# Performance work log

Hardware: AMD Instinct MI355X
Metric: run time of the kernel (lower is better)

Reference implementation:

```python
import jax, jax.numpy as jnp
import numpy as np

N = 50000   # total nodes across batched graphs
E = 800000  # total edges
F = 30      # input node features
G = 256     # number of graphs in the disjoint batch
CH = [128, 64, 32]
N_LABELS = 2


def setup_inputs() -> dict:
    key = jax.random.key(0)
    ks = jax.random.split(key, 16)
    x = jax.random.normal(ks[0], (N, F), dtype=jnp.float32)
    edge_weight = jax.random.uniform(ks[1], (E,), dtype=jnp.float32)
    edge_row = jax.random.randint(ks[2], (E,), 0, N, dtype=jnp.int32)
    edge_col = jax.random.randint(ks[3], (E,), 0, N, dtype=jnp.int32)
    seg = jnp.sort(jax.random.randint(ks[4], (N,), 0, G, dtype=jnp.int32))
    # GCSConv params: out = A @ (x W1) + x W2 + b, per layer
    dims = [F] + CH
    params = {}
    kk = 5
    for l in range(3):
        fin, fout = dims[l], dims[l + 1]
        s = 1.0 / np.sqrt(fin)
        params[f"w1_{l+1}"] = jax.random.uniform(ks[kk], (fin, fout), minval=-s, maxval=s, dtype=jnp.float32); kk += 1
        params[f"w2_{l+1}"] = jax.random.uniform(ks[kk], (fin, fout), minval=-s, maxval=s, dtype=jnp.float32); kk += 1
        params[f"b_{l+1}"] = jnp.zeros((fout,), dtype=jnp.float32)
    sd = 1.0 / np.sqrt(CH[-1])
    params["wd"] = jax.random.uniform(ks[kk], (CH[-1], N_LABELS), minval=-sd, maxval=sd, dtype=jnp.float32)
    params["bd"] = jnp.zeros((N_LABELS,), dtype=jnp.float32)
    return {"x": x, "edge_weight": edge_weight, "edge_row": edge_row,
            "edge_col": edge_col, "seg": seg, **params}


def _gcs_conv(x, ew, er, ec, w1, w2, b):
    # spektral GCSConv: relu(A @ (x W1) + x W2 + b) with sparse A in COO form
    h = x @ w1                                   # [N, Fout]
    msgs = ew[:, None] * h[ec]                   # gather along edges [E, Fout]
    agg = jax.ops.segment_sum(msgs, er, num_segments=N)  # SpMM scatter [N, Fout]
    return jax.nn.relu(agg + x @ w2 + b)


def reference(x, edge_weight, edge_row, edge_col, seg,
              w1_1, w2_1, b_1, w1_2, w2_2, b_2, w1_3, w2_3, b_3, wd, bd):
    h = _gcs_conv(x, edge_weight, edge_row, edge_col, w1_1, w2_1, b_1)
    h = _gcs_conv(h, edge_weight, edge_row, edge_col, w1_2, w2_2, b_2)
    h = _gcs_conv(h, edge_weight, edge_row, edge_col, w1_3, w2_3, b_3)
    # GlobalAvgPool: segment mean over graph ids
    sums = jax.ops.segment_sum(h, seg, num_segments=G)               # [G, 32]
    cnts = jax.ops.segment_sum(jnp.ones((N,), h.dtype), seg, num_segments=G)
    pooled = sums / jnp.maximum(cnts, 1.0)[:, None]
    return jax.nn.softmax(pooled @ wd + bd, axis=-1)                 # [G, 2]
```

## Files before the change

kernel.cpp:

```cpp
#include <hip/hip_runtime.h>
#include <hip/hip_fp16.h>

#define N_NODES 50000
#define N_EDGES 800000
#define N_GRAPHS 256
#define NCB 196
#define CHUNK 3125
#define MBLK 782

typedef _Float16 f16x8 __attribute__((ext_vector_type(8)));
typedef float    f32x4 __attribute__((ext_vector_type(4)));

__global__ __launch_bounds__(256)
void hist_prep(const int* __restrict__ ER, const float* __restrict__ X,
               const int* __restrict__ SEG,
               const float* __restrict__ W1, const float* __restrict__ W2,
               const float* __restrict__ W12, const float* __restrict__ W22,
               const float* __restrict__ W13, const float* __restrict__ W23,
               int* __restrict__ ghist, __half* __restrict__ XPh,
               int* __restrict__ start,
               __half* __restrict__ W1f, __half* __restrict__ W2f,
               __half* __restrict__ W3f)
{
    int b = blockIdx.x;
    int t = threadIdx.x;
    if (b < 256) {
        __shared__ int h[NCB];
        for (int i = t; i < NCB; i += 256) h[i] = 0;
        __syncthreads();
        int lo = b * CHUNK, hi = lo + CHUNK;
        for (int e = lo + t; e < hi; e += 256) atomicAdd(&h[ER[e] >> 8], 1);
        __syncthreads();
        for (int i = t; i < NCB; i += 256) ghist[i * 256 + b] = h[i];
        return;
    }
    int bid = b - 256;
    if (bid < 6250) {
        int idx = bid * 256 + t;
        int n = idx >> 5;
        int c = idx & 31;
        float v = (c < 30) ? X[n * 30 + c] : 0.f;
        XPh[(size_t)n * 32 + c] = __float2half(v);
    } else if (bid < 6446) {
        int n = (bid - 6250) * 256 + t;
        if (n >= N_NODES) return;
        int g = SEG[n];
        int gprev = (n == 0) ? -1 : SEG[n - 1];
        for (int gg = gprev + 1; gg <= g; ++gg) start[gg] = n;
        if (n == N_NODES - 1)
            for (int gg = g + 1; gg <= N_GRAPHS; ++gg) start[gg] = N_NODES;
    } else {
        int idx = (bid - 6446) * 256 + t;
        if (idx < 8192) {
            int i = idx & 7, c = (idx >> 3) & 15, g = (idx >> 7) & 3;
            int s = (idx >> 9) & 1, n = idx >> 10;
            int k = s * 32 + g * 8 + i, col = n * 16 + c;
            float w = 0.f;
            if (k < 30) w = W1[k * 128 + col];
            else if (k >= 32 && k < 62) w = W2[(k - 32) * 128 + col];
            W1f[idx] = __float2half(w);
        } else if (idx < 24576) {
            int o = idx - 8192;
            int i = o & 7, c = (o >> 3) & 15, g = (o >> 7) & 3;
            int s = (o >> 9) & 3, n = o >> 11;
            int k = s * 32 + g * 8 + i, col = n * 16 + c;
            float w = (col < 64) ? W12[k * 64 + col] : W22[k * 64 + col - 64];
            W2f[o] = __float2half(w);
        } else {
            int o = idx - 24576;
            int i = o & 7, c = (o >> 3) & 15, g = (o >> 7) & 3;
            int s = (o >> 9) & 1, n = o >> 10;
            int k = s * 32 + g * 8 + i, col = n * 16 + c;
            float w = (col < 32) ? W13[k * 32 + col] : W23[k * 32 + col - 32];
            W3f[o] = __float2half(w);
        }
    }
}

__global__ __launch_bounds__(256)
void scan1(int* __restrict__ ghist, int* __restrict__ bsum)
{
    __shared__ int s[256];
    int t = threadIdx.x, b = blockIdx.x;
    int i = b * 256 + t;
    int v = ghist[i];
    s[t] = v;
    __syncthreads();
    for (int off = 1; off < 256; off <<= 1) {
        int u = (t >= off) ? s[t - off] : 0;
        __syncthreads();
        s[t] += u;
        __syncthreads();
    }
    ghist[i] = s[t] - v;
    if (t == 255) bsum[b] = s[255];
}

__global__ __launch_bounds__(256)
void c_scatter(const int* __restrict__ ER, const int* __restrict__ EC,
               const float* __restrict__ EW, const int* __restrict__ ghist,
               const int* __restrict__ bsum, unsigned int* __restrict__ tmp_sd,
               __half* __restrict__ tmp_w)
{
    __shared__ int s[256];
    __shared__ int cur[NCB];
    int t = threadIdx.x, blk = blockIdx.x;
    int v = (t < NCB) ? bsum[t] : 0;
    s[t] = v;
    __syncthreads();
    for (int off = 1; off < 256; off <<= 1) {
        int u = (t >= off) ? s[t - off] : 0;
        __syncthreads();
        s[t] += u;
        __syncthreads();
    }
    if (t < NCB) cur[t] = (s[t] - v) + ghist[t * 256 + blk];
    __syncthreads();
    int lo = blk * CHUNK, hi = lo + CHUNK;
    for (int e = lo + t; e < hi; e += 256) {
        int d = ER[e];
        int pos = atomicAdd(&cur[d >> 8], 1);
        tmp_sd[pos] = (unsigned int)EC[e] | ((unsigned int)(d & 255) << 16);
        tmp_w[pos] = __float2half(EW[e]);
    }
}

__device__ __forceinline__ void fma8h(float4& a0, float4& a1, float w,
                                      const uint4& raw)
{
    const __half2* hp = (const __half2*)&raw;
    float2 f0 = __half22float2(hp[0]);
    float2 f1 = __half22float2(hp[1]);
    float2 f2 = __half22float2(hp[2]);
    float2 f3 = __half22float2(hp[3]);
    a0.x = fmaf(w, f0.x, a0.x); a0.y = fmaf(w, f0.y, a0.y);
    a0.z = fmaf(w, f1.x, a0.z); a0.w = fmaf(w, f1.y, a0.w);
    a1.x = fmaf(w, f2.x, a1.x); a1.y = fmaf(w, f2.y, a1.y);
    a1.z = fmaf(w, f3.x, a1.z); a1.w = fmaf(w, f3.y, a1.w);
}

__device__ __forceinline__ unsigned int relu2(unsigned int u)
{
    unsigned int lo = (u & 0x8000u)     ? 0u : (u & 0x0000FFFFu);
    unsigned int hi = (u & 0x80000000u) ? 0u : (u & 0xFFFF0000u);
    return lo | hi;
}

__global__ __launch_bounds__(512)
void bsort_aggx(const unsigned int* __restrict__ tmp_sd, const __half* __restrict__ tmp_w,
                const int* __restrict__ bsum, const __half* __restrict__ XPh,
                unsigned int* __restrict__ packed, int* __restrict__ rowptr,
                __half* __restrict__ CIa)
{
    __shared__ int s[256];
    __shared__ int hist[256];
    __shared__ int cur[256];
    __shared__ int r0arr[257];
    int t = threadIdx.x, b = blockIdx.x;

    if (t < 256) s[t] = (t < NCB) ? bsum[t] : 0;
    __syncthreads();
    for (int off = 1; off < 256; off <<= 1) {
        int u = 0;
        if (t < 256 && t >= off) u = s[t - off];
        __syncthreads();
        if (t < 256) s[t] += u;
        __syncthreads();
    }
    int cntb = bsum[b];
    int base = s[b] - cntb;
    int end  = base + cntb;
    __syncthreads();

    if (t < 256) hist[t] = 0;
    __syncthreads();
    for (int j = base + t; j < end; j += 512)
        atomicAdd(&hist[(tmp_sd[j] >> 16) & 255], 1);
    __syncthreads();
    int hv = 0;
    if (t < 256) { hv = hist[t]; s[t] = hv; }
    __syncthreads();
    for (int off = 1; off < 256; off <<= 1) {
        int u = 0;
        if (t < 256 && t >= off) u = s[t - off];
        __syncthreads();
        if (t < 256) s[t] += u;
        __syncthreads();
    }
    if (t < 256) {
        int excl = s[t] - hv;
        int n = b * 256 + t;
        if (n < N_NODES) rowptr[n] = base + excl;
        if (b == NCB - 1 && t == 0) rowptr[N_NODES] = N_EDGES;
        r0arr[t] = base + excl;
        cur[t] = base + excl;
        if (t == 0) r0arr[256] = end;
    }
    __syncthreads();
    for (int j = base + t; j < end; j += 512) {
        unsigned int sd = tmp_sd[j];
        unsigned short hb = __half_as_ushort(tmp_w[j]);
        int pos = atomicAdd(&cur[(sd >> 16) & 255], 1);
        packed[pos] = (sd & 0xFFFF) | ((unsigned int)hb << 16);
    }
    __syncthreads();

    #pragma unroll
    for (int pass = 0; pass < 2; ++pass) {
        int local = pass * 128 + (t >> 2);
        int q = t & 3;
        int n = b * 256 + local;
        if (n < N_NODES) {
            int r0 = r0arr[local], r1 = r0arr[local + 1];
            float4 acc0 = make_float4(0.f, 0.f, 0.f, 0.f);
            float4 acc1 = make_float4(0.f, 0.f, 0.f, 0.f);
            int j = r0;
            for (; j + 3 < r1; j += 4) {
                unsigned int ra = packed[j],     rb = packed[j + 1];
                unsigned int rc = packed[j + 2], rd = packed[j + 3];
                uint4 rawa = *(const uint4*)(XPh + (size_t)(ra & 0xFFFF) * 32 + q * 8);
                uint4 rawb = *(const uint4*)(XPh + (size_t)(rb & 0xFFFF) * 32 + q * 8);
                uint4 rawc = *(const uint4*)(XPh + (size_t)(rc & 0xFFFF) * 32 + q * 8);
                uint4 rawd = *(const uint4*)(XPh + (size_t)(rd & 0xFFFF) * 32 + q * 8);
                float wa = __half2float(__ushort_as_half((unsigned short)(ra >> 16)));
                float wb = __half2float(__ushort_as_half((unsigned short)(rb >> 16)));
                float wc = __half2float(__ushort_as_half((unsigned short)(rc >> 16)));
                float wd = __half2float(__ushort_as_half((unsigned short)(rd >> 16)));
                fma8h(acc0, acc1, wa, rawa);
                fma8h(acc0, acc1, wb, rawb);
                fma8h(acc0, acc1, wc, rawc);
                fma8h(acc0, acc1, wd, rawd);
            }
            for (; j < r1; ++j) {
                unsigned int r = packed[j];
                uint4 raw = *(const uint4*)(XPh + (size_t)(r & 0xFFFF) * 32 + q * 8);
                float w = __half2float(__ushort_as_half((unsigned short)(r >> 16)));
                fma8h(acc0, acc1, w, raw);
            }
            __half2 hb2[4];
            hb2[0] = __float22half2_rn(make_float2(acc0.x, acc0.y));
            hb2[1] = __float22half2_rn(make_float2(acc0.z, acc0.w));
            hb2[2] = __float22half2_rn(make_float2(acc1.x, acc1.y));
            hb2[3] = __float22half2_rn(make_float2(acc1.z, acc1.w));
            *(uint4*)(CIa + (size_t)n * 32 + q * 8) = *(uint4*)&hb2[0];
        }
    }
}

__global__ __launch_bounds__(256)
void dense12_mfma(const __half* __restrict__ CIa, const __half* __restrict__ XPh,
                  const __half* __restrict__ W1f, const float* __restrict__ B1,
                  const __half* __restrict__ W2f, const float* __restrict__ B2,
                  __half* __restrict__ H2h, __half* __restrict__ A2h)
{
    __shared__ __align__(16) __half As[64 * 72];
    __shared__ __align__(16) __half Hs[64 * 136];
    const int tid = threadIdx.x;
    const int m0 = blockIdx.x * 64;
    const int lane = tid & 63;
    const int w  = tid >> 6;
    const int lr = lane & 15;
    const int lg = lane >> 4;

    for (int idx = tid; idx < 512; idx += 256) {
        int row = idx >> 3, c8 = idx & 7;
        int gm = m0 + row;
        uint4 v = make_uint4(0, 0, 0, 0);
        if (gm < N_NODES) {
            const __half* src = (c8 < 4) ? (CIa + (size_t)gm * 32 + c8 * 8)
                                         : (XPh + (size_t)gm * 32 + (c8 - 4) * 8);
            v = *(const uint4*)src;
        }
        *(uint4*)(As + row * 72 + c8 * 8) = v;
    }
    __syncthreads();

    f32x4 acc[4][2];
    #pragma unroll
    for (int m = 0; m < 4; ++m)
        #pragma unroll
        for (int j = 0; j < 2; ++j)
            acc[m][j] = (f32x4){0.f, 0.f, 0.f, 0.f};

    #pragma unroll
    for (int s = 0; s < 2; ++s) {
        f16x8 a[4];
        #pragma unroll
        for (int m = 0; m < 4; ++m)
            a[m] = *(const f16x8*)(As + (m * 16 + lr) * 72 + s * 32 + lg * 8);
        #pragma unroll
        for (int j = 0; j < 2; ++j) {
            const int n = 2 * w + j;
            f16x8 b = *(const f16x8*)(W1f + (((n * 2 + s) * 4 + lg) * 16 + lr) * 8);
            #pragma unroll
            for (int m = 0; m < 4; ++m)
                acc[m][j] = __builtin_amdgcn_mfma_f32_16x16x32_f16(a[m], b, acc[m][j], 0, 0, 0);
        }
    }

    #pragma unroll
    for (int j = 0; j < 2; ++j) {
        const int n = 2 * w + j;
        const float bias = B1[n * 16 + lr];
        #pragma unroll
        for (int m = 0; m < 4; ++m)
            #pragma unroll
            for (int r = 0; r < 4; ++r) {
                float v = fmaxf(acc[m][j][r] + bias, 0.f);
                Hs[(m * 16 + lg * 4 + r) * 136 + n * 16 + lr] = __float2half(v);
            }
    }
    __syncthreads();

    f32x4 acc2[4][2];
    #pragma unroll
    for (int m = 0; m < 4; ++m)
        #pragma unroll
        for (int j = 0; j < 2; ++j)
            acc2[m][j] = (f32x4){0.f, 0.f, 0.f, 0.f};

    #pragma unroll
    for (int s = 0; s < 4; ++s) {
        f16x8 a[4];
        #pragma unroll
        for (int m = 0; m < 4; ++m)
            a[m] = *(const f16x8*)(Hs + (m * 16 + lr) * 136 + s * 32 + lg * 8);
        #pragma unroll
        for (int j = 0; j < 2; ++j) {
            const int n = 2 * w + j;
            f16x8 b = *(const f16x8*)(W2f + (((n * 4 + s) * 4 + lg) * 16 + lr) * 8);
            #pragma unroll
            for (int m = 0; m < 4; ++m)
                acc2[m][j] = __builtin_amdgcn_mfma_f32_16x16x32_f16(a[m], b, acc2[m][j], 0, 0, 0);
        }
    }
    __syncthreads();

    #pragma unroll
    for (int j = 0; j < 2; ++j) {
        const int n = 2 * w + j;
        const float bias = (n >= 4) ? B2[(n - 4) * 16 + lr] : 0.f;
        #pragma unroll
        for (int m = 0; m < 4; ++m)
            #pragma unroll
            for (int r = 0; r < 4; ++r)
                Hs[(m * 16 + lg * 4 + r) * 136 + n * 16 + lr] =
                    __float2half(acc2[m][j][r] + bias);
    }
    __syncthreads();

    for (int idx = tid; idx < 1024; idx += 256) {
        int row = idx >> 4, c8 = idx & 15;
        int gm = m0 + row;
        if (gm < N_NODES) {
            uint4 v = *(const uint4*)(Hs + row * 136 + c8 * 8);
            if (c8 < 8) *(uint4*)(H2h + (size_t)gm * 64 + c8 * 8) = v;
            else        *(uint4*)(A2h + (size_t)gm * 64 + (c8 - 8) * 8) = v;
        }
    }
}

__global__ __launch_bounds__(256)
void dense3_mfma(const __half* __restrict__ X, const __half* __restrict__ W3f,
                 const float* __restrict__ B3, __half* __restrict__ H3h,
                 __half* __restrict__ B2h)
{
    __shared__ __align__(16) __half As[64 * 72];
    __shared__ __align__(16) __half Os[64 * 72];
    const int tid = threadIdx.x;
    const int m0 = blockIdx.x * 64;
    const int lane = tid & 63;
    const int w  = tid >> 6;
    const int lr = lane & 15;
    const int lg = lane >> 4;

    for (int idx = tid; idx < 512; idx += 256) {
        int row = idx >> 3, c8 = idx & 7;
        int gm = m0 + row;
        uint4 v = make_uint4(0, 0, 0, 0);
        if (gm < N_NODES) v = *(const uint4*)(X + (size_t)gm * 64 + c8 * 8);
        v.x = relu2(v.x); v.y = relu2(v.y); v.z = relu2(v.z); v.w = relu2(v.w);
        *(uint4*)(As + row * 72 + c8 * 8) = v;
    }
    __syncthreads();

    f32x4 acc[4];
    #pragma unroll
    for (int m = 0; m < 4; ++m) acc[m] = (f32x4){0.f, 0.f, 0.f, 0.f};

    #pragma unroll
    for (int s = 0; s < 2; ++s) {
        f16x8 b = *(const f16x8*)(W3f + (((w * 2 + s) * 4 + lg) * 16 + lr) * 8);
        #pragma unroll
        for (int m = 0; m < 4; ++m) {
            f16x8 a = *(const f16x8*)(As + (m * 16 + lr) * 72 + s * 32 + lg * 8);
            acc[m] = __builtin_amdgcn_mfma_f32_16x16x32_f16(a, b, acc[m], 0, 0, 0);
        }
    }

    const float bias = (w >= 2) ? B3[(w - 2) * 16 + lr] : 0.f;
    #pragma unroll
    for (int m = 0; m < 4; ++m)
        #pragma unroll
        for (int r = 0; r < 4; ++r)
            Os[(m * 16 + lg * 4 + r) * 72 + w * 16 + lr] =
                __float2half(acc[m][r] + bias);
    __syncthreads();

    for (int idx = tid; idx < 512; idx += 256) {
        int row = idx >> 3, c8 = idx & 7;
        int gm = m0 + row;
        if (gm < N_NODES) {
            uint4 v = *(const uint4*)(Os + row * 72 + c8 * 8);
            if (c8 < 4) *(uint4*)(H3h + (size_t)gm * 32 + c8 * 8) = v;
            else        *(uint4*)(B2h + (size_t)gm * 32 + (c8 - 4) * 8) = v;
        }
    }
}

template<int FOUT>
__global__ __launch_bounds__(256)
void spmm_h(const __half* __restrict__ H, const int* __restrict__ rowptr,
            const unsigned int* __restrict__ packed, __half* __restrict__ AGGh)
{
    constexpr int T = FOUT / 8;
    int tid = threadIdx.x;
    int local = tid / T;
    int q = tid % T;
    int n = blockIdx.x * (256 / T) + local;
    if (n >= N_NODES) return;
    int r0 = rowptr[n], r1 = rowptr[n + 1];
    __half* ap = AGGh + (size_t)n * FOUT + q * 8;
    float4 acc0, acc1;
    {
        uint4 raw = *(const uint4*)ap;
        const __half2* hp = (const __half2*)&raw;
        float2 f0 = __half22float2(hp[0]);
        float2 f1 = __half22float2(hp[1]);
        float2 f2 = __half22float2(hp[2]);
        float2 f3 = __half22float2(hp[3]);
        acc0 = make_float4(f0.x, f0.y, f1.x, f1.y);
        acc1 = make_float4(f2.x, f2.y, f3.x, f3.y);
    }
    int j = r0;
    for (; j + 3 < r1; j += 4) {
        unsigned int ra = packed[j],     rb = packed[j + 1];
        unsigned int rc = packed[j + 2], rd = packed[j + 3];
        uint4 rawa = *(const uint4*)(H + (size_t)(ra & 0xFFFF) * FOUT + q * 8);
        uint4 rawb = *(const uint4*)(H + (size_t)(rb & 0xFFFF) * FOUT + q * 8);
        uint4 rawc = *(const uint4*)(H + (size_t)(rc & 0xFFFF) * FOUT + q * 8);
        uint4 rawd = *(const uint4*)(H + (size_t)(rd & 0xFFFF) * FOUT + q * 8);
        float wa = __half2float(__ushort_as_half((unsigned short)(ra >> 16)));
        float wb = __half2float(__ushort_as_half((unsigned short)(rb >> 16)));
        float wc = __half2float(__ushort_as_half((unsigned short)(rc >> 16)));
        float wd = __half2float(__ushort_as_half((unsigned short)(rd >> 16)));
        fma8h(acc0, acc1, wa, rawa);
        fma8h(acc0, acc1, wb, rawb);
        fma8h(acc0, acc1, wc, rawc);
        fma8h(acc0, acc1, wd, rawd);
    }
    for (; j < r1; ++j) {
        unsigned int r = packed[j];
        uint4 raw = *(const uint4*)(H + (size_t)(r & 0xFFFF) * FOUT + q * 8);
        float w = __half2float(__ushort_as_half((unsigned short)(r >> 16)));
        fma8h(acc0, acc1, w, raw);
    }
    __half2 hb[4];
    hb[0] = __float22half2_rn(make_float2(acc0.x, acc0.y));
    hb[1] = __float22half2_rn(make_float2(acc0.z, acc0.w));
    hb[2] = __float22half2_rn(make_float2(acc1.x, acc1.y));
    hb[3] = __float22half2_rn(make_float2(acc1.z, acc1.w));
    *(uint4*)ap = *(uint4*)&hb[0];
}

__global__ __launch_bounds__(256)
void pool_kernel(const __half* __restrict__ H, const int* __restrict__ start,
                 const float* __restrict__ WD, const float* __restrict__ BD,
                 float* __restrict__ OUT)
{
    __shared__ float red[8][33];
    int g = blockIdx.x;
    int s = start[g], e = start[g + 1];
    int q = threadIdx.x & 31;
    int lane = threadIdx.x >> 5;
    float acc = 0.f;
    for (int n = s + lane; n < e; n += 8)
        acc += fmaxf(__half2float(H[(size_t)n * 32 + q]), 0.f);
    red[lane][q] = acc;
    __syncthreads();
    if (threadIdx.x < 32) {
        float v = 0.f;
        #pragma unroll
        for (int i = 0; i < 8; ++i) v += red[i][q];
        float inv = (e > s) ? 1.0f / (float)(e - s) : 1.0f;
        float p = v * inv;
        float p0 = p * WD[q * 2 + 0];
        float p1 = p * WD[q * 2 + 1];
        #pragma unroll
        for (int off = 16; off; off >>= 1) {
            p0 += __shfl_down(p0, off, 32);
            p1 += __shfl_down(p1, off, 32);
        }
        if (q == 0) {
            float l0 = p0 + BD[0], l1 = p1 + BD[1];
            float m = fmaxf(l0, l1);
            float e0 = expf(l0 - m), e1 = expf(l1 - m);
            float si = 1.0f / (e0 + e1);
            OUT[g * 2 + 0] = e0 * si;
            OUT[g * 2 + 1] = e1 * si;
        }
    }
}

extern "C" void kernel_launch(void* const* d_in, const int* in_sizes, int n_in,
                              void* d_out, int out_size, void* d_ws, size_t ws_size,
                              hipStream_t stream)
{
    const float* x    = (const float*)d_in[0];
    const float* ew   = (const float*)d_in[1];
    const int*   er   = (const int*)d_in[2];
    const int*   ec   = (const int*)d_in[3];
    const int*   seg  = (const int*)d_in[4];
    const float* w1_1 = (const float*)d_in[5];
    const float* w2_1 = (const float*)d_in[6];
    const float* b_1  = (const float*)d_in[7];
    const float* w1_2 = (const float*)d_in[8];
    const float* w2_2 = (const float*)d_in[9];
    const float* b_2  = (const float*)d_in[10];
    const float* w1_3 = (const float*)d_in[11];
    const float* w2_3 = (const float*)d_in[12];
    const float* b_3  = (const float*)d_in[13];
    const float* wd   = (const float*)d_in[14];
    const float* bd   = (const float*)d_in[15];

    float* ws = (float*)d_ws;
    int*   IW = (int*)d_ws;
    __half* XPh    = (__half*)ws;
    __half* CIa    = (__half*)(ws + 800000);
    unsigned int* tmp_sd = (unsigned int*)(ws + 1600000);
    __half* tmp_w  = (__half*)(ws + 2400000);
    __half* H2h    = (__half*)(ws + 3200000);
    __half* A2h    = (__half*)(ws + 4800000);
    __half* H3h    = (__half*)(ws + 6400000);
    __half* B2h    = (__half*)(ws + 7200000);
    unsigned int* packed = (unsigned int*)(IW + 8000000);
    int*    rowptr = IW + 9000000;
    int*    ghist  = IW + 9060000;
    int*    bsum   = IW + 9115000;
    int*    start  = IW + 9120000;
    __half* W1f    = (__half*)(ws + 9125000);
    __half* W2f    = (__half*)(ws + 9130000);
    __half* W3f    = (__half*)(ws + 9139000);

    dim3 blk(256);

    hist_prep<<<dim3(256 + 6558), blk, 0, stream>>>(er, x, seg, w1_1, w2_1,
                                                    w1_2, w2_2, w1_3, w2_3,
                                                    ghist, XPh, start,
                                                    W1f, W2f, W3f);
    scan1<<<dim3(NCB), blk, 0, stream>>>(ghist, bsum);
    c_scatter<<<dim3(256), blk, 0, stream>>>(er, ec, ew, ghist, bsum, tmp_sd, tmp_w);
    bsort_aggx<<<dim3(NCB), dim3(512), 0, stream>>>(tmp_sd, tmp_w, bsum, XPh,
                                                    packed, rowptr, CIa);

    dense12_mfma<<<dim3(MBLK), blk, 0, stream>>>(CIa, XPh, W1f, b_1,
                                                 W2f, b_2, H2h, A2h);
    spmm_h<64><<<dim3((N_NODES + 31) / 32), blk, 0, stream>>>(H2h, rowptr, packed, A2h);
    dense3_mfma<<<dim3(MBLK), blk, 0, stream>>>(A2h, W3f, b_3, H3h, B2h);
    spmm_h<32><<<dim3(MBLK), blk, 0, stream>>>(H3h, rowptr, packed, B2h);

    pool_kernel<<<dim3(N_GRAPHS), blk, 0, stream>>>(B2h, start, wd, bd, (float*)d_out);
}
```

Baseline: 180.4 us.

## Split layer-2 SpMM into two 32-wide passes and fuse final SpMM with pooling

Layer-2 dense outputs are written as two 32-column halves, and the 64-wide SpMM is replaced by two 32-wide SpMM launches, which shrinks the gather footprint per pass. The final layer-3 SpMM is fused with global average pooling. It applies ReLU, reduces into per-block shared-memory graph bins, then does global float atomics into a zeroed partial-sum buffer, and a single-block head kernel computes the mean, dense layer and softmax. This removes the B2h write/read and the separate pool pass, but adds float atomics (non-deterministic summation order) and one extra kernel launch.

```diff
diff --git a/kernel.cpp b/kernel.cpp
--- a/kernel.cpp
+++ b/kernel.cpp
@@ -20,7 +20,7 @@
                int* __restrict__ ghist, __half* __restrict__ XPh,
                int* __restrict__ start,
                __half* __restrict__ W1f, __half* __restrict__ W2f,
-               __half* __restrict__ W3f)
+               __half* __restrict__ W3f, float* __restrict__ PS)
 {
     int b = blockIdx.x;
     int t = threadIdx.x;
@@ -49,7 +49,7 @@
         for (int gg = gprev + 1; gg <= g; ++gg) start[gg] = n;
         if (n == N_NODES - 1)
             for (int gg = g + 1; gg <= N_GRAPHS; ++gg) start[gg] = N_NODES;
-    } else {
+    } else if (bid < 6558) {
         int idx = (bid - 6446) * 256 + t;
         if (idx < 8192) {
             int i = idx & 7, c = (idx >> 3) & 15, g = (idx >> 7) & 3;
@@ -74,6 +74,9 @@
             float w = (col < 32) ? W13[k * 32 + col] : W23[k * 32 + col - 32];
             W3f[o] = __float2half(w);
         }
+    } else {
+        int idx = (bid - 6558) * 256 + t;
+        PS[idx] = 0.f;
     }
 }
 
@@ -251,7 +254,8 @@
 void dense12_mfma(const __half* __restrict__ CIa, const __half* __restrict__ XPh,
                   const __half* __restrict__ W1f, const float* __restrict__ B1,
                   const __half* __restrict__ W2f, const float* __restrict__ B2,
-                  __half* __restrict__ H2h, __half* __restrict__ A2h)
+                  __half* __restrict__ H2a, __half* __restrict__ H2b,
+                  __half* __restrict__ A2a, __half* __restrict__ A2b)
 {
     __shared__ __align__(16) __half As[64 * 72];
     __shared__ __align__(16) __half Hs[64 * 136];
@@ -354,14 +358,21 @@
         int gm = m0 + row;
         if (gm < N_NODES) {
             uint4 v = *(const uint4*)(Hs + row * 136 + c8 * 8);
-            if (c8 < 8) *(uint4*)(H2h + (size_t)gm * 64 + c8 * 8) = v;
-            else        *(uint4*)(A2h + (size_t)gm * 64 + (c8 - 8) * 8) = v;
-        }
-    }
-}
-
-__global__ __launch_bounds__(256)
-void dense3_mfma(const __half* __restrict__ X, const __half* __restrict__ W3f,
+            __half* dst;
+            switch (c8 >> 2) {
+            case 0:  dst = H2a; break;
+            case 1:  dst = H2b; break;
+            case 2:  dst = A2a; break;
+            default: dst = A2b; break;
+            }
+            *(uint4*)(dst + (size_t)gm * 32 + (c8 & 3) * 8) = v;
+        }
+    }
+}
+
+__global__ __launch_bounds__(256)
+void dense3_mfma(const __half* __restrict__ A2a, const __half* __restrict__ A2b,
+                 const __half* __restrict__ W3f,
                  const float* __restrict__ B3, __half* __restrict__ H3h,
                  __half* __restrict__ B2h)
 {
@@ -378,7 +389,11 @@
         int row = idx >> 3, c8 = idx & 7;
         int gm = m0 + row;
         uint4 v = make_uint4(0, 0, 0, 0);
-        if (gm < N_NODES) v = *(const uint4*)(X + (size_t)gm * 64 + c8 * 8);
+        if (gm < N_NODES) {
+            const __half* src = (c8 < 4) ? (A2a + (size_t)gm * 32 + c8 * 8)
+                                         : (A2b + (size_t)gm * 32 + (c8 - 4) * 8);
+            v = *(const uint4*)src;
+        }
         v.x = relu2(v.x); v.y = relu2(v.y); v.z = relu2(v.z); v.w = relu2(v.w);
         *(uint4*)(As + row * 72 + c8 * 8) = v;
     }
@@ -474,42 +489,99 @@
 }
 
 __global__ __launch_bounds__(256)
-void pool_kernel(const __half* __restrict__ H, const int* __restrict__ start,
+void spmm_pool(const __half* __restrict__ H, const int* __restrict__ rowptr,
+               const unsigned int* __restrict__ packed,
+               const __half* __restrict__ Bse, const int* __restrict__ SEG,
+               float* __restrict__ PS)
+{
+    __shared__ float ps[65][32];
+    int tid = threadIdx.x;
+    int local = tid >> 2;
+    int q = tid & 3;
+    int n0 = blockIdx.x * 64;
+    int n = n0 + local;
+    for (int i = tid; i < 65 * 32; i += 256) ((float*)ps)[i] = 0.f;
+    __syncthreads();
+    int g0 = SEG[n0];
+    if (n < N_NODES) {
+        int g = SEG[n];
+        int r0 = rowptr[n], r1 = rowptr[n + 1];
+        float4 acc0, acc1;
+        {
+            uint4 raw = *(const uint4*)(Bse + (size_t)n * 32 + q * 8);
+            const __half2* hp = (const __half2*)&raw;
+            float2 f0 = __half22float2(hp[0]);
+            float2 f1 = __half22float2(hp[1]);
+            float2 f2 = __half22float2(hp[2]);
+            float2 f3 = __half22float2(hp[3]);
+            acc0 = make_float4(f0.x, f0.y, f1.x, f1.y);
+            acc1 = make_float4(f2.x, f2.y, f3.x, f3.y);
+        }
+        int j = r0;
+        for (; j + 3 < r1; j += 4) {
+            unsigned int ra = packed[j],     rb = packed[j + 1];
+            unsigned int rc = packed[j + 2], rd = packed[j + 3];
+            uint4 rawa = *(const uint4*)(H + (size_t)(ra & 0xFFFF) * 32 + q * 8);
+            uint4 rawb = *(const uint4*)(H + (size_t)(rb & 0xFFFF) * 32 + q * 8);
+            uint4 rawc = *(const uint4*)(H + (size_t)(rc & 0xFFFF) * 32 + q * 8);
+            uint4 rawd = *(const uint4*)(H + (size_t)(rd & 0xFFFF) * 32 + q * 8);
+            float wa = __half2float(__ushort_as_half((unsigned short)(ra >> 16)));
+            float wb = __half2float(__ushort_as_half((unsigned short)(rb >> 16)));
+            float wc = __half2float(__ushort_as_half((unsigned short)(rc >> 16)));
+            float wd = __half2float(__ushort_as_half((unsigned short)(rd >> 16)));
+            fma8h(acc0, acc1, wa, rawa);
+            fma8h(acc0, acc1, wb, rawb);
+            fma8h(acc0, acc1, wc, rawc);
+            fma8h(acc0, acc1, wd, rawd);
+        }
+        for (; j < r1; ++j) {
+            unsigned int r = packed[j];
+            uint4 raw = *(const uint4*)(H + (size_t)(r & 0xFFFF) * 32 + q * 8);
+            float w = __half2float(__ushort_as_half((unsigned short)(r >> 16)));
+            fma8h(acc0, acc1, w, raw);
+        }
+        float* dst = &ps[g - g0][q * 8];
+        atomicAdd(&dst[0], fmaxf(acc0.x, 0.f));
+        atomicAdd(&dst[1], fmaxf(acc0.y, 0.f));
+        atomicAdd(&dst[2], fmaxf(acc0.z, 0.f));
+        atomicAdd(&dst[3], fmaxf(acc0.w, 0.f));
+        atomicAdd(&dst[4], fmaxf(acc1.x, 0.f));
+        atomicAdd(&dst[5], fmaxf(acc1.y, 0.f));
+        atomicAdd(&dst[6], fmaxf(acc1.z, 0.f));
+        atomicAdd(&dst[7], fmaxf(acc1.w, 0.f));
+    }
+    __syncthreads();
+    int nlast = n0 + 63;
+    if (nlast >= N_NODES) nlast = N_NODES - 1;
+    int span = SEG[nlast] - g0 + 1;
+    for (int i = tid; i < span * 32; i += 256) {
+        float v = ps[i >> 5][i & 31];
+        if (v != 0.f)
+            atomicAdd(&PS[(size_t)(g0 + (i >> 5)) * 32 + (i & 31)], v);
+    }
+}
+
+__global__ __launch_bounds__(256)
+void head_kernel(const float* __restrict__ PS, const int* __restrict__ start,
                  const float* __restrict__ WD, const float* __restrict__ BD,
                  float* __restrict__ OUT)
 {
-    __shared__ float red[8][33];
-    int g = blockIdx.x;
+    int g = threadIdx.x;
     int s = start[g], e = start[g + 1];
-    int q = threadIdx.x & 31;
-    int lane = threadIdx.x >> 5;
-    float acc = 0.f;
-    for (int n = s + lane; n < e; n += 8)
-        acc += fmaxf(__half2float(H[(size_t)n * 32 + q]), 0.f);
-    red[lane][q] = acc;
-    __syncthreads();
-    if (threadIdx.x < 32) {
-        float v = 0.f;
-        #pragma unroll
-        for (int i = 0; i < 8; ++i) v += red[i][q];
-        float inv = (e > s) ? 1.0f / (float)(e - s) : 1.0f;
-        float p = v * inv;
-        float p0 = p * WD[q * 2 + 0];
-        float p1 = p * WD[q * 2 + 1];
-        #pragma unroll
-        for (int off = 16; off; off >>= 1) {
-            p0 += __shfl_down(p0, off, 32);
-            p1 += __shfl_down(p1, off, 32);
-        }
-        if (q == 0) {
-            float l0 = p0 + BD[0], l1 = p1 + BD[1];
-            float m = fmaxf(l0, l1);
-            float e0 = expf(l0 - m), e1 = expf(l1 - m);
-            float si = 1.0f / (e0 + e1);
-            OUT[g * 2 + 0] = e0 * si;
-            OUT[g * 2 + 1] = e1 * si;
-        }
-    }
+    float inv = (e > s) ? 1.0f / (float)(e - s) : 1.0f;
+    float l0 = 0.f, l1 = 0.f;
+    #pragma unroll
+    for (int j = 0; j < 32; ++j) {
+        float p = PS[g * 32 + j] * inv;
+        l0 = fmaf(p, WD[j * 2 + 0], l0);
+        l1 = fmaf(p, WD[j * 2 + 1], l1);
+    }
+    l0 += BD[0]; l1 += BD[1];
+    float m = fmaxf(l0, l1);
+    float e0 = expf(l0 - m), e1 = expf(l1 - m);
+    float si = 1.0f / (e0 + e1);
+    OUT[g * 2 + 0] = e0 * si;
+    OUT[g * 2 + 1] = e1 * si;
 }
 
 extern "C" void kernel_launch(void* const* d_in, const int* in_sizes, int n_in,
@@ -539,8 +611,10 @@
     __half* CIa    = (__half*)(ws + 800000);
     unsigned int* tmp_sd = (unsigned int*)(ws + 1600000);
     __half* tmp_w  = (__half*)(ws + 2400000);
-    __half* H2h    = (__half*)(ws + 3200000);
-    __half* A2h    = (__half*)(ws + 4800000);
+    __half* H2a    = (__half*)(ws + 3200000);
+    __half* H2b    = (__half*)(ws + 4000000);
+    __half* A2a    = (__half*)(ws + 4800000);
+    __half* A2b    = (__half*)(ws + 5600000);
     __half* H3h    = (__half*)(ws + 6400000);
     __half* B2h    = (__half*)(ws + 7200000);
     unsigned int* packed = (unsigned int*)(IW + 8000000);
@@ -551,23 +625,24 @@
     __half* W1f    = (__half*)(ws + 9125000);
     __half* W2f    = (__half*)(ws + 9130000);
     __half* W3f    = (__half*)(ws + 9139000);
+    float*  PS     = ws + 9145000;
 
     dim3 blk(256);
 
-    hist_prep<<<dim3(256 + 6558), blk, 0, stream>>>(er, x, seg, w1_1, w2_1,
+    hist_prep<<<dim3(256 + 6590), blk, 0, stream>>>(er, x, seg, w1_1, w2_1,
                                                     w1_2, w2_2, w1_3, w2_3,
                                                     ghist, XPh, start,
-                                                    W1f, W2f, W3f);
+                                                    W1f, W2f, W3f, PS);
     scan1<<<dim3(NCB), blk, 0, stream>>>(ghist, bsum);
     c_scatter<<<dim3(256), blk, 0, stream>>>(er, ec, ew, ghist, bsum, tmp_sd, tmp_w);
     bsort_aggx<<<dim3(NCB), dim3(512), 0, stream>>>(tmp_sd, tmp_w, bsum, XPh,
                                                     packed, rowptr, CIa);
 
     dense12_mfma<<<dim3(MBLK), blk, 0, stream>>>(CIa, XPh, W1f, b_1,
-                                                 W2f, b_2, H2h, A2h);
-    spmm_h<64><<<dim3((N_NODES + 31) / 32), blk, 0, stream>>>(H2h, rowptr, packed, A2h);
-    dense3_mfma<<<dim3(MBLK), blk, 0, stream>>>(A2h, W3f, b_3, H3h, B2h);
-    spmm_h<32><<<dim3(MBLK), blk, 0, stream>>>(H3h, rowptr, packed, B2h);
-
-    pool_kernel<<<dim3(N_GRAPHS), blk, 0, stream>>>(B2h, start, wd, bd, (float*)d_out);
-}
+                                                 W2f, b_2, H2a, H2b, A2a, A2b);
+    spmm_h<32><<<dim3(MBLK), blk, 0, stream>>>(H2a, rowptr, packed, A2a);
+    spmm_h<32><<<dim3(MBLK), blk, 0, stream>>>(H2b, rowptr, packed, A2b);
+    dense3_mfma<<<dim3(MBLK), blk, 0, stream>>>(A2a, A2b, w1_3 ? W3f : W3f, b_3, H3h, B2h);
+    spmm_pool<<<dim3(MBLK), blk, 0, stream>>>(H3h, rowptr, packed, B2h, seg, PS);
+    head_kernel<<<dim3(1), blk, 0, stream>>>(PS, start, wd, bd, (float*)d_out);
+}
```

After: 190.5 us. +5.6%, slower.

## Split each row's edge range across two thread groups in SpMM, widen bsort block

Applied to the files above, without the earlier changes.

The SpMM kernels now assign two thread groups per node, each summing half of the node's edge range, then combine the partials through shared memory before writing the fp16 result. Blocks grow to 512 threads while keeping the same nodes per block. The bucket-sort/aggregation kernel moves to 1024-thread blocks so the per-node aggregation runs in one pass instead of two. This aims to raise memory-level parallelism for the gather-heavy SpMM, at the cost of an extra shared-memory reduction, a block barrier, and larger blocks that may lower occupancy.

```diff
diff --git a/kernel.cpp b/kernel.cpp
--- a/kernel.cpp
+++ b/kernel.cpp
@@ -146,7 +146,7 @@
     return lo | hi;
 }
 
-__global__ __launch_bounds__(512)
+__global__ __launch_bounds__(1024)
 void bsort_aggx(const unsigned int* __restrict__ tmp_sd, const __half* __restrict__ tmp_w,
                 const int* __restrict__ bsum, const __half* __restrict__ XPh,
                 unsigned int* __restrict__ packed, int* __restrict__ rowptr,
@@ -174,7 +174,7 @@
 
     if (t < 256) hist[t] = 0;
     __syncthreads();
-    for (int j = base + t; j < end; j += 512)
+    for (int j = base + t; j < end; j += 1024)
         atomicAdd(&hist[(tmp_sd[j] >> 16) & 255], 1);
     __syncthreads();
     int hv = 0;
@@ -197,7 +197,7 @@
         if (t == 0) r0arr[256] = end;
     }
     __syncthreads();
-    for (int j = base + t; j < end; j += 512) {
+    for (int j = base + t; j < end; j += 1024) {
         unsigned int sd = tmp_sd[j];
         unsigned short hb = __half_as_ushort(tmp_w[j]);
         int pos = atomicAdd(&cur[(sd >> 16) & 255], 1);
@@ -205,9 +205,8 @@
     }
     __syncthreads();
 
-    #pragma unroll
-    for (int pass = 0; pass < 2; ++pass) {
-        int local = pass * 128 + (t >> 2);
+    {
+        int local = t >> 2;
         int q = t & 3;
         int n = b * 256 + local;
         if (n < N_NODES) {
@@ -419,58 +418,79 @@
 }
 
 template<int FOUT>
-__global__ __launch_bounds__(256)
-void spmm_h(const __half* __restrict__ H, const int* __restrict__ rowptr,
-            const unsigned int* __restrict__ packed, __half* __restrict__ AGGh)
+__global__ __launch_bounds__(512)
+void spmm_split(const __half* __restrict__ H, const int* __restrict__ rowptr,
+                const unsigned int* __restrict__ packed, __half* __restrict__ AGGh)
 {
     constexpr int T = FOUT / 8;
+    constexpr int NPB = 512 / (2 * T);
+    __shared__ float part[NPB][FOUT + 4];
     int tid = threadIdx.x;
-    int local = tid / T;
-    int q = tid % T;
-    int n = blockIdx.x * (256 / T) + local;
-    if (n >= N_NODES) return;
-    int r0 = rowptr[n], r1 = rowptr[n + 1];
+    int local = tid / (2 * T);
+    int rem = tid % (2 * T);
+    int s = rem / T;
+    int q = rem % T;
+    int n = blockIdx.x * NPB + local;
+    bool valid = (n < N_NODES);
+    float4 acc0 = make_float4(0.f, 0.f, 0.f, 0.f);
+    float4 acc1 = make_float4(0.f, 0.f, 0.f, 0.f);
     __half* ap = AGGh + (size_t)n * FOUT + q * 8;
-    float4 acc0, acc1;
-    {
-        uint4 raw = *(const uint4*)ap;
-        const __half2* hp = (const __half2*)&raw;
-        float2 f0 = __half22float2(hp[0]);
-        float2 f1 = __half22float2(hp[1]);
-        float2 f2 = __half22float2(hp[2]);
-        float2 f3 = __half22float2(hp[3]);
-        acc0 = make_float4(f0.x, f0.y, f1.x, f1.y);
-        acc1 = make_float4(f2.x, f2.y, f3.x, f3.y);
-    }
-    int j = r0;
-    for (; j + 3 < r1; j += 4) {
-        unsigned int ra = packed[j],     rb = packed[j + 1];
-        unsigned int rc = packed[j + 2], rd = packed[j + 3];
-        uint4 rawa = *(const uint4*)(H + (size_t)(ra & 0xFFFF) * FOUT + q * 8);
-        uint4 rawb = *(const uint4*)(H + (size_t)(rb & 0xFFFF) * FOUT + q * 8);
-        uint4 rawc = *(const uint4*)(H + (size_t)(rc & 0xFFFF) * FOUT + q * 8);
-        uint4 rawd = *(const uint4*)(H + (size_t)(rd & 0xFFFF) * FOUT + q * 8);
-        float wa = __half2float(__ushort_as_half((unsigned short)(ra >> 16)));
-        float wb = __half2float(__ushort_as_half((unsigned short)(rb >> 16)));
-        float wc = __half2float(__ushort_as_half((unsigned short)(rc >> 16)));
-        float wd = __half2float(__ushort_as_half((unsigned short)(rd >> 16)));
-        fma8h(acc0, acc1, wa, rawa);
-        fma8h(acc0, acc1, wb, rawb);
-        fma8h(acc0, acc1, wc, rawc);
-        fma8h(acc0, acc1, wd, rawd);
-    }
-    for (; j < r1; ++j) {
-        unsigned int r = packed[j];
-        uint4 raw = *(const uint4*)(H + (size_t)(r & 0xFFFF) * FOUT + q * 8);
-        float w = __half2float(__ushort_as_half((unsigned short)(r >> 16)));
-        fma8h(acc0, acc1, w, raw);
-    }
-    __half2 hb[4];
-    hb[0] = __float22half2_rn(make_float2(acc0.x, acc0.y));
-    hb[1] = __float22half2_rn(make_float2(acc0.z, acc0.w));
-    hb[2] = __float22half2_rn(make_float2(acc1.x, acc1.y));
-    hb[3] = __float22half2_rn(make_float2(acc1.z, acc1.w));
-    *(uint4*)ap = *(uint4*)&hb[0];
+    if (valid) {
+        int r0 = rowptr[n], r1 = rowptr[n + 1];
+        int mid = (r0 + r1) >> 1;
+        int lo = s ? mid : r0;
+        int hi = s ? r1 : mid;
+        if (s == 0) {
+            uint4 raw = *(const uint4*)ap;
+            const __half2* hp = (const __half2*)&raw;
+            float2 f0 = __half22float2(hp[0]);
+            float2 f1 = __half22float2(hp[1]);
+            float2 f2 = __half22float2(hp[2]);
+            float2 f3 = __half22float2(hp[3]);
+            acc0 = make_float4(f0.x, f0.y, f1.x, f1.y);
+            acc1 = make_float4(f2.x, f2.y, f3.x, f3.y);
+        }
+        int j = lo;
+        for (; j + 3 < hi; j += 4) {
+            unsigned int ra = packed[j],     rb = packed[j + 1];
+            unsigned int rc = packed[j + 2], rd = packed[j + 3];
+            uint4 rawa = *(const uint4*)(H + (size_t)(ra & 0xFFFF) * FOUT + q * 8);
+            uint4 rawb = *(const uint4*)(H + (size_t)(rb & 0xFFFF) * FOUT + q * 8);
+            uint4 rawc = *(const uint4*)(H + (size_t)(rc & 0xFFFF) * FOUT + q * 8);
+            uint4 rawd = *(const uint4*)(H + (size_t)(rd & 0xFFFF) * FOUT + q * 8);
+            float wa = __half2float(__ushort_as_half((unsigned short)(ra >> 16)));
+            float wb = __half2float(__ushort_as_half((unsigned short)(rb >> 16)));
+            float wc = __half2float(__ushort_as_half((unsigned short)(rc >> 16)));
+            float wd = __half2float(__ushort_as_half((unsigned short)(rd >> 16)));
+            fma8h(acc0, acc1, wa, rawa);
+            fma8h(acc0, acc1, wb, rawb);
+            fma8h(acc0, acc1, wc, rawc);
+            fma8h(acc0, acc1, wd, rawd);
+        }
+        for (; j < hi; ++j) {
+            unsigned int r = packed[j];
+            uint4 raw = *(const uint4*)(H + (size_t)(r & 0xFFFF) * FOUT + q * 8);
+            float w = __half2float(__ushort_as_half((unsigned short)(r >> 16)));
+            fma8h(acc0, acc1, w, raw);
+        }
+    }
+    if (s == 1) {
+        *(float4*)&part[local][q * 8 + 0] = acc0;
+        *(float4*)&part[local][q * 8 + 4] = acc1;
+    }
+    __syncthreads();
+    if (s == 0 && valid) {
+        float4 p0 = *(float4*)&part[local][q * 8 + 0];
+        float4 p1 = *(float4*)&part[local][q * 8 + 4];
+        acc0.x += p0.x; acc0.y += p0.y; acc0.z += p0.z; acc0.w += p0.w;
+        acc1.x += p1.x; acc1.y += p1.y; acc1.z += p1.z; acc1.w += p1.w;
+        __half2 hb[4];
+        hb[0] = __float22half2_rn(make_float2(acc0.x, acc0.y));
+        hb[1] = __float22half2_rn(make_float2(acc0.z, acc0.w));
+        hb[2] = __float22half2_rn(make_float2(acc1.x, acc1.y));
+        hb[3] = __float22half2_rn(make_float2(acc1.z, acc1.w));
+        *(uint4*)ap = *(uint4*)&hb[0];
+    }
 }
 
 __global__ __launch_bounds__(256)
@@ -560,14 +580,15 @@
                                                     W1f, W2f, W3f);
     scan1<<<dim3(NCB), blk, 0, stream>>>(ghist, bsum);
     c_scatter<<<dim3(256), blk, 0, stream>>>(er, ec, ew, ghist, bsum, tmp_sd, tmp_w);
-    bsort_aggx<<<dim3(NCB), dim3(512), 0, stream>>>(tmp_sd, tmp_w, bsum, XPh,
-                                                    packed, rowptr, CIa);
+    bsort_aggx<<<dim3(NCB), dim3(1024), 0, stream>>>(tmp_sd, tmp_w, bsum, XPh,
+                                                     packed, rowptr, CIa);
 
     dense12_mfma<<<dim3(MBLK), blk, 0, stream>>>(CIa, XPh, W1f, b_1,
                                                  W2f, b_2, H2h, A2h);
-    spmm_h<64><<<dim3((N_NODES + 31) / 32), blk, 0, stream>>>(H2h, rowptr, packed, A2h);
+    spmm_split<64><<<dim3((N_NODES + 31) / 32), dim3(512), 0, stream>>>(H2h, rowptr,
+                                                                        packed, A2h);
     dense3_mfma<<<dim3(MBLK), blk, 0, stream>>>(A2h, W3f, b_3, H3h, B2h);
-    spmm_h<32><<<dim3(MBLK), blk, 0, stream>>>(H3h, rowptr, packed, B2h);
+    spmm_split<32><<<dim3(MBLK), dim3(512), 0, stream>>>(H3h, rowptr, packed, B2h);
 
     pool_kernel<<<dim3(N_GRAPHS), blk, 0, stream>>>(B2h, start, wd, bd, (float*)d_out);
 }
```

Result: faster. 176.7 us (-2.0%).
